# Optimization experiments

Hardware: AMD Instinct MI355X
Metric: run time of the kernel (lower is better)

The kernel has to match this reference:

```python
import jax, jax.numpy as jnp
import numpy as np

B, D, S = 16384, 1024, 1024

def _layernorm(x, g, b, eps=1e-5):
    mu = jnp.mean(x, axis=-1, keepdims=True)
    var = jnp.mean(jnp.square(x - mu), axis=-1, keepdims=True)
    return (x - mu) * jax.lax.rsqrt(var + eps) * g + b

def setup_inputs() -> dict:
    key = jax.random.key(0)
    ks = jax.random.split(key, 8)
    inv = lambda n: 1.0 / np.sqrt(n)
    return {
        "x": jax.random.normal(ks[0], (B, D), jnp.float32),
        "s_prev0": jax.random.normal(ks[1], (B, S), jnp.float32),
        "s_prev1": jax.random.normal(ks[2], (B, S), jnp.float32),
        "Wi": jax.random.uniform(ks[3], (4 * S, D), jnp.float32, -inv(D), inv(D)),
        "Ws": jax.random.uniform(ks[4], (4 * S, 2 * S), jnp.float32, -inv(2 * S), inv(2 * S)),
        "lni_g": jnp.ones((4 * S,), jnp.float32),
        "lni_b": jnp.zeros((4 * S,), jnp.float32),
        "lns_g": jnp.ones((4 * S,), jnp.float32),
        "lns_b": jnp.zeros((4 * S,), jnp.float32),
        "lnh_g": jnp.ones((S,), jnp.float32),
        "lnh_b": jnp.zeros((S,), jnp.float32),
    }

def reference(x, s_prev0, s_prev1, Wi, Ws, lni_g, lni_b, lns_g, lns_b, lnh_g, lnh_b):
    s = jnp.concatenate([s_prev0, s_prev1], axis=-1)  # [B, 2S]
    igates = _layernorm(x @ Wi.T, lni_g, lni_b)        # [B, 4S]
    sgates = _layernorm(s @ Ws.T, lns_g, lns_b)        # [B, 4S]
    gates = igates + sgates
    r_inv, i, n, l = jnp.split(gates, 4, axis=1)
    s_n = sgates[:, 2 * S:3 * S]
    l = jax.nn.sigmoid(l)
    r_inv = jax.nn.sigmoid(r_inv)
    i = jax.nn.sigmoid(i)
    n = jnp.tanh(n - r_inv * s_n)
    h = n + i * (l * s_prev0 + (1.0 - l) * s_prev1 - n)
    return _layernorm(h, lnh_g, lnh_b)
```

## Files before the change

### kernel.cpp

```cpp
#include <hip/hip_runtime.h>
#include <cstdint>


typedef unsigned short ushort_t;
typedef __attribute__((ext_vector_type(8))) __bf16 bf16x8;
typedef __attribute__((ext_vector_type(4))) float f32x4;

__device__ __forceinline__ ushort_t f2b(float f) {
    unsigned u = __float_as_uint(f);
    unsigned r = (u + 0x7fffu + ((u >> 16) & 1u)) >> 16;
    return (ushort_t)r;
}
__device__ __forceinline__ float b2f(ushort_t u) {
    return __uint_as_float(((unsigned)u) << 16);
}

__device__ __forceinline__ void gl_lds16(const void* g, void* l) {
    __builtin_amdgcn_global_load_lds(
        (const __attribute__((address_space(1))) unsigned int*)(uintptr_t)g,
        (__attribute__((address_space(3))) unsigned int*)(uintptr_t)l,
        16, 0, 0);
}

#define LOG2E 1.4426950408889634f
__device__ __forceinline__ float fexp2(float x) { return __builtin_amdgcn_exp2f(x); }
__device__ __forceinline__ float frcp(float x)  { return __builtin_amdgcn_rcpf(x); }
__device__ __forceinline__ float fsigmoid(float x) {
    return frcp(1.f + fexp2(-LOG2E * x));
}
__device__ __forceinline__ float ftanh(float y) {
    return 1.f - 2.f * frcp(1.f + fexp2((2.f * LOG2E) * y));
}

__global__ __launch_bounds__(256) void cast_bf16(const float* __restrict__ src,
                                                 ushort_t* __restrict__ dst, long n) {
    long i = ((long)blockIdx.x * 256 + threadIdx.x) * 4;
    if (i + 3 < n) {
        float4 v = *(const float4*)(src + i);
        ushort4 u;
        u.x = f2b(v.x); u.y = f2b(v.y); u.z = f2b(v.z); u.w = f2b(v.w);
        *(ushort4*)(dst + i) = u;
    }
}

__global__ __launch_bounds__(256) void cast_concat(const float* __restrict__ s0,
                                                   const float* __restrict__ s1,
                                                   ushort_t* __restrict__ dst) {
    long i = ((long)blockIdx.x * 256 + threadIdx.x) * 4;
    long row = i >> 11;
    int  col = (int)(i & 2047);
    const float* src = (col < 1024) ? (s0 + row * 1024 + col)
                                    : (s1 + row * 1024 + (col - 1024));
    float4 v = *(const float4*)src;
    ushort4 u;
    u.x = f2b(v.x); u.y = f2b(v.y); u.z = f2b(v.z); u.w = f2b(v.w);
    *(ushort4*)(dst + i) = u;
}


__device__ __forceinline__ void stage2(const char* s0, const char* s1,
                                       int d0, int d1, char* ldsbase,
                                       int kt, int NT) {
    if (kt < NT) {
        long kb = (long)kt << 7;
        char* lb = ldsbase + ((kt & 1) << 15);
        gl_lds16(s0 + kb, lb + d0);
        gl_lds16(s1 + kb, lb + d1);
    }
}

__global__ __launch_bounds__(512, 2) void gemm_bt(const ushort_t* __restrict__ A,
                                                  const ushort_t* __restrict__ W,
                                                  ushort_t* __restrict__ C,
                                                  int M, int N, int K) {
    (void)M;
    __shared__ __align__(16) ushort_t As[2][256 * 64];
    __shared__ __align__(16) ushort_t Bs[2][256 * 64];

    const int NT   = K >> 6;
    const int t    = threadIdx.x;
    const int lane = t & 63;
    const int w    = t >> 6;
    const int gm   = w >> 2;
    const int gn   = w & 3;
    const int gb   = gn & 1;
    const int wm   = gm << 7;
    const int wn   = gn << 6;

    const int nwg  = gridDim.x;
    const int cpx  = nwg >> 3;
    const int orig = blockIdx.x;
    const int wgid = (orig & 7) * cpx + (orig >> 3);
    const int NXB  = N >> 8;
    const int bx   = wgid % NXB;
    const int by   = wgid / NXB;
    const int bm0  = by << 8;
    const int bn0  = bx << 8;

    const int u0r = t >> 3;
    const int chb = (t & 7) << 4;
    const int cbs = chb ^ ((u0r & 7) << 4);
    const int ur0 = u0r, ur1 = 64 + u0r;

    #define AER(ur) ((ur) < 64 ? (ur) : (ur) + 128)
    #define ALR(ur) ((ur) + 64)
    #define BER(ur) (((((ur) >> 5) >> 1) << 7) + ((((ur) >> 5) & 1) * 96) + ((ur) & 31))
    #define BLR(ur) ((ur) + 32 + (((ur) >> 6) << 6))

    const char* sAe0 = (const char*)(A + (long)(bm0 + AER(ur0)) * K) + cbs;
    const char* sAe1 = (const char*)(A + (long)(bm0 + AER(ur1)) * K) + cbs;
    const char* sAl0 = (const char*)(A + (long)(bm0 + ALR(ur0)) * K) + cbs;
    const char* sAl1 = (const char*)(A + (long)(bm0 + ALR(ur1)) * K) + cbs;
    const char* sBe0 = (const char*)(W + (long)(bn0 + BER(ur0)) * K) + cbs;
    const char* sBe1 = (const char*)(W + (long)(bn0 + BER(ur1)) * K) + cbs;
    const char* sBl0 = (const char*)(W + (long)(bn0 + BLR(ur0)) * K) + cbs;
    const char* sBl1 = (const char*)(W + (long)(bn0 + BLR(ur1)) * K) + cbs;

    const int dAe0 = AER(ur0) * 128 + chb, dAe1 = AER(ur1) * 128 + chb;
    const int dAl0 = ALR(ur0) * 128 + chb, dAl1 = ALR(ur1) * 128 + chb;
    const int dBe0 = BER(ur0) * 128 + chb, dBe1 = BER(ur1) * 128 + chb;
    const int dBl0 = BLR(ur0) * 128 + chb, dBl1 = BLR(ur1) * 128 + chb;

    char* Abase = (char*)&As[0][0];
    char* Bbase = (char*)&Bs[0][0];

    const int ml   = lane & 15;
    const int g    = lane >> 4;
    const int rsw  = (lane & 7) << 4;
    const int kc0  = ((g << 4)) ^ rsw;
    const int kc1  = (64 | (g << 4)) ^ rsw;
    const int arow = (wm + ml) << 7;
    const int brow = (wn + ml) << 7;

    f32x4 acc[4][4][2];
#pragma unroll
    for (int q = 0; q < 4; q++)
#pragma unroll
        for (int ii = 0; ii < 4; ii++)
#pragma unroll
            for (int jj = 0; jj < 2; jj++)
                acc[q][ii][jj] = (f32x4){0.f, 0.f, 0.f, 0.f};

    stage2(sAe0, sAe1, dAe0, dAe1, Abase, 0, NT);
    stage2(sAl0, sAl1, dAl0, dAl1, Abase, 0, NT);
    stage2(sBe0, sBe1, dBe0, dBe1, Bbase, 0, NT);
    stage2(sBl0, sBl1, dBl0, dBl1, Bbase, 0, NT);
    stage2(sAe0, sAe1, dAe0, dAe1, Abase, 1, NT);
    stage2(sBe0, sBe1, dBe0, dBe1, Bbase, 1, NT);
    asm volatile("s_waitcnt vmcnt(4)" ::: "memory");
    __builtin_amdgcn_s_barrier();

    for (int kt = 0; kt < NT; ++kt) {
        const char* Ab = Abase + ((kt & 1) << 15);
        const char* Bb = Bbase + ((kt & 1) << 15);
        bf16x8 af[4][2];
        bf16x8 bfr[2][2][2];
#pragma unroll
        for (int q = 0; q < 4; ++q) {
            const int qm = (q >> 1) ^ gm;
            const int qn = (q & 1) ^ gb;

            if (q < 2) {
#pragma unroll
                for (int jj = 0; jj < 2; jj++) {
                    const int ro = brow + ((qn << 1) + jj) * 2048;
                    bfr[q][jj][0] = *(const bf16x8*)(Bb + ro + kc0);
                    bfr[q][jj][1] = *(const bf16x8*)(Bb + ro + kc1);
                }
            }
            if ((q & 1) == 0) {
#pragma unroll
                for (int ii = 0; ii < 4; ii++) {
                    const int ro = arow + ((qm << 2) + ii) * 2048;
                    af[ii][0] = *(const bf16x8*)(Ab + ro + kc0);
                    af[ii][1] = *(const bf16x8*)(Ab + ro + kc1);
                }
            }

            if (q == 0)      stage2(sAl0, sAl1, dAl0, dAl1, Abase, kt + 1, NT);
            else if (q == 1) stage2(sBl0, sBl1, dBl0, dBl1, Bbase, kt + 1, NT);
            else if (q == 3) {
                stage2(sAe0, sAe1, dAe0, dAe1, Abase, kt + 2, NT);
                stage2(sBe0, sBe1, dBe0, dBe1, Bbase, kt + 2, NT);
                if (kt < NT - 2) asm volatile("s_waitcnt vmcnt(4)" ::: "memory");
                else             asm volatile("s_waitcnt vmcnt(0)" ::: "memory");
            }
            __builtin_amdgcn_s_barrier();
            __builtin_amdgcn_s_setprio(1);
#pragma unroll
            for (int ii = 0; ii < 4; ii++)
#pragma unroll
                for (int jj = 0; jj < 2; jj++)
#pragma unroll
                    for (int kh = 0; kh < 2; kh++)
                        acc[q][ii][jj] = __builtin_amdgcn_mfma_f32_16x16x32_bf16(
                            af[ii][kh], bfr[q & 1][jj][kh], acc[q][ii][jj], 0, 0, 0);
            __builtin_amdgcn_s_setprio(0);
            __builtin_amdgcn_s_barrier();
        }
    }

    const int quad = (lane >> 4) << 2;
#pragma unroll
    for (int q = 0; q < 4; ++q) {
        const int qm = (q >> 1) ^ gm;
        const int qn = (q & 1) ^ gb;
#pragma unroll
        for (int ii = 0; ii < 4; ii++)
#pragma unroll
            for (int jj = 0; jj < 2; jj++)
#pragma unroll
                for (int r = 0; r < 4; r++) {
                    const int cm = bm0 + wm + ((qm << 2) + ii) * 16 + quad + r;
                    const int cn = bn0 + wn + ((qn << 1) + jj) * 16 + ml;
                    C[(long)cm * N + cn] = f2b(acc[q][ii][jj][r]);
                }
    }
}

__global__ __launch_bounds__(256) void fuse_ln(const ushort_t* __restrict__ M1,
                                               const ushort_t* __restrict__ M2,
                                               const float* __restrict__ p0,
                                               const float* __restrict__ p1,
                                               const float* __restrict__ lni_g,
                                               const float* __restrict__ lni_b,
                                               const float* __restrict__ lns_g,
                                               const float* __restrict__ lns_b,
                                               const float* __restrict__ lnh_g,
                                               const float* __restrict__ lnh_b,
                                               float* __restrict__ out) {
    const int row = blockIdx.x;
    const int t   = threadIdx.x;
    const long base = (long)row * 4096;

    __shared__ float sred[16];
    __shared__ float stats[8];

    float v1[4][4], v2[4][4];
    float s1 = 0.f, q1 = 0.f, s2 = 0.f, q2 = 0.f;
#pragma unroll
    for (int q = 0; q < 4; q++) {
        ushort4 a = *(const ushort4*)(M1 + base + q * 1024 + t * 4);
        ushort4 b = *(const ushort4*)(M2 + base + q * 1024 + t * 4);
        const ushort_t* ap = (const ushort_t*)&a;
        const ushort_t* bp = (const ushort_t*)&b;
#pragma unroll
        for (int j = 0; j < 4; j++) {
            float f1 = b2f(ap[j]); v1[q][j] = f1; s1 += f1; q1 += f1 * f1;
            float f2 = b2f(bp[j]); v2[q][j] = f2; s2 += f2; q2 += f2 * f2;
        }
    }
    float r4[4] = {s1, q1, s2, q2};
#pragma unroll
    for (int off = 32; off > 0; off >>= 1) {
#pragma unroll
        for (int i = 0; i < 4; i++) r4[i] += __shfl_down(r4[i], off, 64);
    }
    if ((t & 63) == 0) {
        int w = t >> 6;
#pragma unroll
        for (int i = 0; i < 4; i++) sred[w * 4 + i] = r4[i];
    }
    __syncthreads();
    if (t == 0) {
        float S1 = 0, Q1 = 0, S2 = 0, Q2 = 0;
        for (int w = 0; w < 4; w++) {
            S1 += sred[w * 4]; Q1 += sred[w * 4 + 1];
            S2 += sred[w * 4 + 2]; Q2 += sred[w * 4 + 3];
        }
        float mu1 = S1 * (1.f / 4096.f), mu2 = S2 * (1.f / 4096.f);
        float var1 = Q1 * (1.f / 4096.f) - mu1 * mu1;
        float var2 = Q2 * (1.f / 4096.f) - mu2 * mu2;
        stats[0] = mu1; stats[1] = rsqrtf(var1 + 1e-5f);
        stats[2] = mu2; stats[3] = rsqrtf(var2 + 1e-5f);
    }
    __syncthreads();
    const float mu1 = stats[0], rs1 = stats[1], mu2 = stats[2], rs2 = stats[3];

    float4 Gi[4], Bi[4], Gs[4], Bs[4];
#pragma unroll
    for (int q = 0; q < 4; q++) {
        Gi[q] = *(const float4*)(lni_g + q * 1024 + t * 4);
        Bi[q] = *(const float4*)(lni_b + q * 1024 + t * 4);
        Gs[q] = *(const float4*)(lns_g + q * 1024 + t * 4);
        Bs[q] = *(const float4*)(lns_b + q * 1024 + t * 4);
    }
    float4 P0 = *(const float4*)(p0 + (long)row * 1024 + t * 4);
    float4 P1 = *(const float4*)(p1 + (long)row * 1024 + t * 4);

    float h[4];
    float sh = 0.f, qh = 0.f;
#pragma unroll
    for (int j = 0; j < 4; j++) {
        float gq[4], snv = 0.f;
#pragma unroll
        for (int q = 0; q < 4; q++) {
            float a = (v1[q][j] - mu1) * rs1 * ((const float*)&Gi[q])[j] + ((const float*)&Bi[q])[j];
            float b = (v2[q][j] - mu2) * rs2 * ((const float*)&Gs[q])[j] + ((const float*)&Bs[q])[j];
            if (q == 2) snv = b;
            gq[q] = a + b;
        }
        float rg = fsigmoid(gq[0]);
        float ig = fsigmoid(gq[1]);
        float lg = fsigmoid(gq[3]);
        float ng = ftanh(gq[2] - rg * snv);
        float pp0 = ((const float*)&P0)[j], pp1 = ((const float*)&P1)[j];
        float hv = ng + ig * (lg * pp0 + (1.f - lg) * pp1 - ng);
        h[j] = hv; sh += hv; qh += hv * hv;
    }
    float r2[2] = {sh, qh};
#pragma unroll
    for (int off = 32; off > 0; off >>= 1) {
#pragma unroll
        for (int i = 0; i < 2; i++) r2[i] += __shfl_down(r2[i], off, 64);
    }
    if ((t & 63) == 0) {
        int w = t >> 6;
        sred[w * 4] = r2[0]; sred[w * 4 + 1] = r2[1];
    }
    __syncthreads();
    if (t == 0) {
        float S = 0, Q = 0;
        for (int w = 0; w < 4; w++) { S += sred[w * 4]; Q += sred[w * 4 + 1]; }
        float mu = S * (1.f / 1024.f);
        float var = Q * (1.f / 1024.f) - mu * mu;
        stats[4] = mu; stats[5] = rsqrtf(var + 1e-5f);
    }
    __syncthreads();
    const float muh = stats[4], rsh = stats[5];

    float4 Gh = *(const float4*)(lnh_g + t * 4);
    float4 Bh = *(const float4*)(lnh_b + t * 4);
    float4 O;
#pragma unroll
    for (int j = 0; j < 4; j++)
        ((float*)&O)[j] = (h[j] - muh) * rsh * ((const float*)&Gh)[j] + ((const float*)&Bh)[j];
    *(float4*)(out + (long)row * 1024 + t * 4) = O;
}

extern "C" void kernel_launch(void* const* d_in, const int* in_sizes, int n_in,
                              void* d_out, int out_size, void* d_ws, size_t ws_size,
                              hipStream_t stream) {
    const float* x     = (const float*)d_in[0];
    const float* s0    = (const float*)d_in[1];
    const float* s1    = (const float*)d_in[2];
    const float* Wi    = (const float*)d_in[3];
    const float* Ws    = (const float*)d_in[4];
    const float* lni_g = (const float*)d_in[5];
    const float* lni_b = (const float*)d_in[6];
    const float* lns_g = (const float*)d_in[7];
    const float* lns_b = (const float*)d_in[8];
    const float* lnh_g = (const float*)d_in[9];
    const float* lnh_b = (const float*)d_in[10];
    float* out = (float*)d_out;

    char* wsb = (char*)d_ws;
    ushort_t* M1  = (ushort_t*)wsb;
    ushort_t* M2  = (ushort_t*)(wsb + (((size_t)128) << 20));
    ushort_t* Wsb = (ushort_t*)wsb;
    ushort_t* sb  = (ushort_t*)d_out;
    ushort_t* xb  = (ushort_t*)d_out;
    ushort_t* Wib = (ushort_t*)((char*)d_out + (((size_t)32) << 20));

    dim3 g(1024);

    cast_concat<<<32768, 256, 0, stream>>>(s0, s1, sb);
    cast_bf16<<<8192, 256, 0, stream>>>(Ws, Wsb, (long)4096 * 2048);
    gemm_bt<<<g, 512, 0, stream>>>(sb, Wsb, M2, 16384, 4096, 2048);
    cast_bf16<<<16384, 256, 0, stream>>>(x, xb, (long)16384 * 1024);
    cast_bf16<<<4096, 256, 0, stream>>>(Wi, Wib, (long)4096 * 1024);
    gemm_bt<<<g, 512, 0, stream>>>(xb, Wib, M1, 16384, 4096, 1024);
    fuse_ln<<<16384, 256, 0, stream>>>(M1, M2, s0, s1, lni_g, lni_b, lns_g,
                                       lns_b, lnh_g, lnh_b, out);
}
```

Before: 758.3 us.

## Software-pipeline LDS fragment reads ahead of MFMA phases in GEMM main loop

Restructures the GEMM k-loop so the LDS fragment reads for the next MFMA phase are issued right after the current phase's MFMAs, including reading the next k-tile's first A/B fragments before the loop iterates. Fragment registers are hoisted out of the loop, and the barriers and vmcnt waits are reordered to match. The aim is to hide LDS read latency behind matrix math. In exchange it adds register pressure and more barriers per k-step, and correctness depends on the next buffer being resident when it is read early.

```diff
diff --git a/kernel.cpp b/kernel.cpp
--- a/kernel.cpp
+++ b/kernel.cpp
@@ -69,6 +69,27 @@
     }
 }
 
+#define MFMA_PHASE(Q, BS)                                                     \
+    _Pragma("unroll") for (int ii = 0; ii < 4; ii++)                          \
+        _Pragma("unroll") for (int jj = 0; jj < 2; jj++)                      \
+            _Pragma("unroll") for (int kh = 0; kh < 2; kh++)                  \
+                acc[Q][ii][jj] = __builtin_amdgcn_mfma_f32_16x16x32_bf16(     \
+                    af[ii][kh], bfr[BS][jj][kh], acc[Q][ii][jj], 0, 0, 0);
+
+#define READ_B(BS, QN, BASE)                                                  \
+    _Pragma("unroll") for (int jj = 0; jj < 2; jj++) {                        \
+        const int ro = brow + (((QN) << 1) + jj) * 2048;                      \
+        bfr[BS][jj][0] = *(const bf16x8*)((BASE) + ro + kc0);                 \
+        bfr[BS][jj][1] = *(const bf16x8*)((BASE) + ro + kc1);                 \
+    }
+
+#define READ_A(QM, BASE)                                                      \
+    _Pragma("unroll") for (int ii = 0; ii < 4; ii++) {                        \
+        const int ro = arow + (((QM) << 2) + ii) * 2048;                      \
+        af[ii][0] = *(const bf16x8*)((BASE) + ro + kc0);                      \
+        af[ii][1] = *(const bf16x8*)((BASE) + ro + kc1);                      \
+    }
+
 __global__ __launch_bounds__(512, 2) void gemm_bt(const ushort_t* __restrict__ A,
                                                   const ushort_t* __restrict__ W,
                                                   ushort_t* __restrict__ C,
@@ -141,6 +162,9 @@
             for (int jj = 0; jj < 2; jj++)
                 acc[q][ii][jj] = (f32x4){0.f, 0.f, 0.f, 0.f};
 
+    bf16x8 af[4][2];
+    bf16x8 bfr[2][2][2];
+
     stage2(sAe0, sAe1, dAe0, dAe1, Abase, 0, NT);
     stage2(sAl0, sAl1, dAl0, dAl1, Abase, 0, NT);
     stage2(sBe0, sBe1, dBe0, dBe1, Bbase, 0, NT);
@@ -149,55 +173,49 @@
     stage2(sBe0, sBe1, dBe0, dBe1, Bbase, 1, NT);
     asm volatile("s_waitcnt vmcnt(4)" ::: "memory");
     __builtin_amdgcn_s_barrier();
+    READ_B(0, gb, Bbase);
+    READ_A(gm, Abase);
 
     for (int kt = 0; kt < NT; ++kt) {
-        const char* Ab = Abase + ((kt & 1) << 15);
-        const char* Bb = Bbase + ((kt & 1) << 15);
-        bf16x8 af[4][2];
-        bf16x8 bfr[2][2][2];
-#pragma unroll
-        for (int q = 0; q < 4; ++q) {
-            const int qm = (q >> 1) ^ gm;
-            const int qn = (q & 1) ^ gb;
-
-            if (q < 2) {
-#pragma unroll
-                for (int jj = 0; jj < 2; jj++) {
-                    const int ro = brow + ((qn << 1) + jj) * 2048;
-                    bfr[q][jj][0] = *(const bf16x8*)(Bb + ro + kc0);
-                    bfr[q][jj][1] = *(const bf16x8*)(Bb + ro + kc1);
-                }
-            }
-            if ((q & 1) == 0) {
-#pragma unroll
-                for (int ii = 0; ii < 4; ii++) {
-                    const int ro = arow + ((qm << 2) + ii) * 2048;
-                    af[ii][0] = *(const bf16x8*)(Ab + ro + kc0);
-                    af[ii][1] = *(const bf16x8*)(Ab + ro + kc1);
-                }
-            }
-
-            if (q == 0)      stage2(sAl0, sAl1, dAl0, dAl1, Abase, kt + 1, NT);
-            else if (q == 1) stage2(sBl0, sBl1, dBl0, dBl1, Bbase, kt + 1, NT);
-            else if (q == 3) {
-                stage2(sAe0, sAe1, dAe0, dAe1, Abase, kt + 2, NT);
-                stage2(sBe0, sBe1, dBe0, dBe1, Bbase, kt + 2, NT);
-                if (kt < NT - 2) asm volatile("s_waitcnt vmcnt(4)" ::: "memory");
-                else             asm volatile("s_waitcnt vmcnt(0)" ::: "memory");
-            }
-            __builtin_amdgcn_s_barrier();
-            __builtin_amdgcn_s_setprio(1);
-#pragma unroll
-            for (int ii = 0; ii < 4; ii++)
-#pragma unroll
-                for (int jj = 0; jj < 2; jj++)
-#pragma unroll
-                    for (int kh = 0; kh < 2; kh++)
-                        acc[q][ii][jj] = __builtin_amdgcn_mfma_f32_16x16x32_bf16(
-                            af[ii][kh], bfr[q & 1][jj][kh], acc[q][ii][jj], 0, 0, 0);
-            __builtin_amdgcn_s_setprio(0);
-            __builtin_amdgcn_s_barrier();
-        }
+        const char* AbT = Abase + ((kt & 1) << 15);
+        const char* BbT = Bbase + ((kt & 1) << 15);
+        const char* AbN = Abase + (((kt + 1) & 1) << 15);
+        const char* BbN = Bbase + (((kt + 1) & 1) << 15);
+
+        stage2(sAl0, sAl1, dAl0, dAl1, Abase, kt + 1, NT);
+        __builtin_amdgcn_s_barrier();
+        __builtin_amdgcn_s_setprio(1);
+        MFMA_PHASE(0, 0);
+        __builtin_amdgcn_s_setprio(0);
+        READ_B(1, 1 ^ gb, BbT);
+        __builtin_amdgcn_s_barrier();
+
+        stage2(sBl0, sBl1, dBl0, dBl1, Bbase, kt + 1, NT);
+        __builtin_amdgcn_s_barrier();
+        __builtin_amdgcn_s_setprio(1);
+        MFMA_PHASE(1, 1);
+        __builtin_amdgcn_s_setprio(0);
+        READ_A(1 ^ gm, AbT);
+        __builtin_amdgcn_s_barrier();
+
+        asm volatile("s_waitcnt vmcnt(4)" ::: "memory");
+        __builtin_amdgcn_s_barrier();
+        __builtin_amdgcn_s_setprio(1);
+        MFMA_PHASE(2, 0);
+        __builtin_amdgcn_s_setprio(0);
+        READ_B(0, gb, BbN);
+        __builtin_amdgcn_s_barrier();
+
+        stage2(sAe0, sAe1, dAe0, dAe1, Abase, kt + 2, NT);
+        stage2(sBe0, sBe1, dBe0, dBe1, Bbase, kt + 2, NT);
+        if (kt < NT - 2) asm volatile("s_waitcnt vmcnt(4)" ::: "memory");
+        else             asm volatile("s_waitcnt vmcnt(0)" ::: "memory");
+        __builtin_amdgcn_s_barrier();
+        __builtin_amdgcn_s_setprio(1);
+        MFMA_PHASE(3, 1);
+        __builtin_amdgcn_s_setprio(0);
+        READ_A(gm, AbN);
+        __builtin_amdgcn_s_barrier();
     }
 
     const int quad = (lane >> 4) << 2;
```

Result: no change. 744.7 us (-1.8%).
